# Performance work log

Hardware: AMD Instinct MI355X
Metric: run time of the kernel (lower is better)

Reference implementation:

```python
import jax, jax.numpy as jnp
import numpy as np

B, L, D = 2, 1024, 1024
H = 16
NL = 2
DFF = 4 * D
EPS = 1e-5
W_SCALE = 0.02


def rmsnorm(x, w):
    # x * rsqrt(mean(x^2, -1) + eps) * w   (computed in fp32 as in the torch code)
    xf = x.astype(jnp.float32)
    n = xf * jax.lax.rsqrt(jnp.mean(xf * xf, axis=-1, keepdims=True) + EPS)
    return n.astype(x.dtype) * w


def setup_inputs() -> dict:
    key = jax.random.key(0)
    ks = jax.random.split(key, 10)
    x = jax.random.normal(ks[0], (B, L, D), dtype=jnp.float32)
    # torch nn.Linear weight layout: [out_features, in_features]; y = x @ W.T + b
    qw = jax.random.normal(ks[1], (NL, D, D), dtype=jnp.float32) * W_SCALE
    kw = jax.random.normal(ks[2], (NL, D, D), dtype=jnp.float32) * W_SCALE
    vw = jax.random.normal(ks[3], (NL, D, D), dtype=jnp.float32) * W_SCALE
    ow = jax.random.normal(ks[4], (NL, D, D), dtype=jnp.float32) * W_SCALE
    pn_w = jnp.ones((NL, D), dtype=jnp.float32)
    ln_w = jnp.ones((NL, D), dtype=jnp.float32)
    fc_w = jax.random.normal(ks[5], (NL, DFF, D), dtype=jnp.float32) * W_SCALE
    fc2_w = jax.random.normal(ks[6], (NL, D, DFF), dtype=jnp.float32) * W_SCALE
    fc2_b = jnp.zeros((NL, D), dtype=jnp.float32)
    return {"x": x, "qw": qw, "kw": kw, "vw": vw, "ow": ow,
            "pn_w": pn_w, "ln_w": ln_w, "fc_w": fc_w, "fc2_w": fc2_w, "fc2_b": fc2_b}


def reference(x, qw, kw, vw, ow, pn_w, ln_w, fc_w, fc2_w, fc2_b):
    d = D // H
    for i in range(NL):
        # --- LinearAttention block (dropout=0 -> identity) ---
        h = rmsnorm(x, pn_w[i])                                   # [B,L,D]
        Q = (h @ qw[i].T).reshape(B, L, H, d)
        K = (h @ kw[i].T).reshape(B, L, H, d)
        V = (h @ vw[i].T).reshape(B, L, H, d)
        # outer-product state per position, cumulated over L (causal linear attn)
        W = jnp.einsum('blhd,blhe->blhde', K, V)                  # [B,L,H,d,d]
        W = jnp.cumsum(W, axis=1)
        a = jnp.einsum('blhd,blhde->blhe', Q, W).reshape(B, L, D)
        x = x + a @ ow[i].T
        # --- MLP block ---
        m = rmsnorm(x, ln_w[i])
        f = jax.nn.gelu(m @ fc_w[i].T, approximate=False)         # torch nn.GELU default = exact
        x = x + f @ fc2_w[i].T + fc2_b[i]
    return x
```

## Files before the change

kernel.cpp:

```cpp
#include <hip/hip_runtime.h>

#define BB 2
#define LL 1024
#define DD 1024
#define HH 16
#define HD 64
#define DFFN 4096
#define MM (BB*LL)
#define QS 3072

using u16 = unsigned short;
typedef __bf16 bf16x8 __attribute__((ext_vector_type(8)));
typedef float f32x4 __attribute__((ext_vector_type(4)));

__device__ __forceinline__ float b2f(u16 u) {
  union { unsigned int i; float f; } v; v.i = ((unsigned int)u) << 16; return v.f;
}
__device__ __forceinline__ u16 f2b(float f) {
  union { float f; unsigned int i; } v; v.f = f;
  unsigned int x = v.i;
  return (u16)((x + 0x7fffu + ((x >> 16) & 1u)) >> 16);
}
__device__ __forceinline__ float gelu_exact(float x) {
  return 0.5f * x * (1.0f + erff(x * 0.70710678118654752f));
}
__device__ __forceinline__ void gl2lds16(const void* g, void* l) {
  __builtin_amdgcn_global_load_lds((const __attribute__((address_space(1))) void*)g,
                                   (__attribute__((address_space(3))) void*)l, 16, 0, 0);
}

__global__ __launch_bounds__(256) void castw_kernel(const float* __restrict__ in,
                                                    u16* __restrict__ out, int n8) {
  int i = blockIdx.x * 256 + threadIdx.x;
  if (i >= n8) return;
  const float4 a = reinterpret_cast<const float4*>(in)[2 * i];
  const float4 b = reinterpret_cast<const float4*>(in)[2 * i + 1];
  uint4 o;
  o.x = (unsigned)f2b(a.x) | ((unsigned)f2b(a.y) << 16);
  o.y = (unsigned)f2b(a.z) | ((unsigned)f2b(a.w) << 16);
  o.z = (unsigned)f2b(b.x) | ((unsigned)f2b(b.y) << 16);
  o.w = (unsigned)f2b(b.z) | ((unsigned)f2b(b.w) << 16);
  reinterpret_cast<uint4*>(out)[i] = o;
}
__global__ __launch_bounds__(256) void castw3_kernel(const float* __restrict__ s0,
                                                     const float* __restrict__ s1,
                                                     const float* __restrict__ s2,
                                                     u16* __restrict__ out, int n8) {
  int i = blockIdx.x * 256 + threadIdx.x;
  if (i >= n8) return;
  const float* in = (blockIdx.y == 0) ? s0 : (blockIdx.y == 1) ? s1 : s2;
  u16* dst = out + (size_t)blockIdx.y * n8 * 8;
  const float4 a = reinterpret_cast<const float4*>(in)[2 * i];
  const float4 b = reinterpret_cast<const float4*>(in)[2 * i + 1];
  uint4 o;
  o.x = (unsigned)f2b(a.x) | ((unsigned)f2b(a.y) << 16);
  o.y = (unsigned)f2b(a.z) | ((unsigned)f2b(a.w) << 16);
  o.z = (unsigned)f2b(b.x) | ((unsigned)f2b(b.y) << 16);
  o.w = (unsigned)f2b(b.z) | ((unsigned)f2b(b.w) << 16);
  reinterpret_cast<uint4*>(dst)[i] = o;
}

__global__ __launch_bounds__(256) void init_out_kernel(float* __restrict__ out,
                                                       const float* __restrict__ resid,
                                                       const float* __restrict__ bias) {
  const int i = blockIdx.x * 256 + threadIdx.x;
  float4 v = reinterpret_cast<const float4*>(resid)[i];
  if (bias != nullptr) {
    const float4 bv = *reinterpret_cast<const float4*>(bias + ((i * 4) & (DD - 1)));
    v.x += bv.x; v.y += bv.y; v.z += bv.z; v.w += bv.w;
  }
  reinterpret_cast<float4*>(out)[i] = v;
}

__global__ __launch_bounds__(256) void rmsnorm_kernel(const float* __restrict__ x,
                                                      const float* __restrict__ w,
                                                      u16* __restrict__ out) {
  const int row = blockIdx.x, t = threadIdx.x;
  const float4 v = reinterpret_cast<const float4*>(x + (size_t)row * DD)[t];
  float ss = v.x*v.x + v.y*v.y + v.z*v.z + v.w*v.w;
  #pragma unroll
  for (int o = 32; o > 0; o >>= 1) ss += __shfl_down(ss, o);
  __shared__ float red[4];
  if ((t & 63) == 0) red[t >> 6] = ss;
  __syncthreads();
  const float inv = rsqrtf((red[0] + red[1] + red[2] + red[3]) * (1.0f / DD) + 1e-5f);
  const float4 wv = reinterpret_cast<const float4*>(w)[t];
  ushort4 o;
  o.x = f2b(v.x * inv * wv.x);
  o.y = f2b(v.y * inv * wv.y);
  o.z = f2b(v.z * inv * wv.z);
  o.w = f2b(v.w * inv * wv.w);
  reinterpret_cast<ushort4*>(out + (size_t)row * DD)[t] = o;
}

template<int BM, int BN, int ACT>
__global__ __launch_bounds__((BM/64)*(BN/64)*64)
void mfma_gemm(const u16* __restrict__ A, const u16* __restrict__ Wb,
               u16* __restrict__ Cb, int N, int K) {
  constexpr int WCOLS = BN / 64;
  constexpr int NW = (BM / 64) * WCOLS;
  constexpr int NT = NW * 64;
  constexpr int IA = BM * 4 / NT, IB = BN * 4 / NT;
  __shared__ u16 As[BM * 32];
  __shared__ u16 Bs[BN * 32];
  const int t = threadIdx.x;
  const int lane = t & 63, w = t >> 6;
  const int wm = (w / WCOLS) * 64, wn = (w % WCOLS) * 64;
  const int m0 = blockIdx.y * BM, n0 = blockIdx.x * BN;
  const int fr = lane & 15, fq = lane >> 4;

  f32x4 acc[4][4] = {};
  for (int kt = 0; kt < K; kt += 32) {
    #pragma unroll
    for (int i = 0; i < IA; i++) {
      const int c = i * NT + t;
      gl2lds16(A + (size_t)(m0 + (c >> 2)) * K + kt + (c & 3) * 8, &As[c * 8]);
    }
    #pragma unroll
    for (int i = 0; i < IB; i++) {
      const int c = i * NT + t;
      gl2lds16(Wb + (size_t)(n0 + (c >> 2)) * K + kt + (c & 3) * 8, &Bs[c * 8]);
    }
    __syncthreads();
    bf16x8 af[4], bfv[4];
    #pragma unroll
    for (int i = 0; i < 4; i++)
      af[i] = *reinterpret_cast<const bf16x8*>(&As[(wm + i * 16 + fr) * 32 + fq * 8]);
    #pragma unroll
    for (int j = 0; j < 4; j++)
      bfv[j] = *reinterpret_cast<const bf16x8*>(&Bs[(wn + j * 16 + fr) * 32 + fq * 8]);
    #pragma unroll
    for (int i = 0; i < 4; i++)
      #pragma unroll
      for (int j = 0; j < 4; j++)
        acc[i][j] = __builtin_amdgcn_mfma_f32_16x16x32_bf16(af[i], bfv[j], acc[i][j], 0, 0, 0);
    __syncthreads();
  }

  #pragma unroll
  for (int i = 0; i < 4; i++)
    #pragma unroll
    for (int j = 0; j < 4; j++)
      #pragma unroll
      for (int r = 0; r < 4; r++) {
        const int row = m0 + wm + i * 16 + fq * 4 + r;
        const int col = n0 + wn + j * 16 + fr;
        float val = acc[i][j][r];
        if (ACT == 1) val = gelu_exact(val);
        Cb[(size_t)row * N + col] = f2b(val);
      }
}

template<int SPLIT>
__global__ __launch_bounds__(256)
void mfma_gemm_sk(const u16* __restrict__ A, const u16* __restrict__ Wb,
                  float* __restrict__ Co, int N, int K) {
  constexpr int BM = 128, BN = 128;
  __shared__ u16 As[BM * 32];
  __shared__ u16 Bs[BN * 32];
  const int t = threadIdx.x;
  const int lane = t & 63, w = t >> 6;
  const int wm = (w >> 1) * 64, wn = (w & 1) * 64;
  const int m0 = blockIdx.y * BM, n0 = blockIdx.x * BN;
  const int fr = lane & 15, fq = lane >> 4;
  const int Kc = K / SPLIT, k0 = blockIdx.z * Kc;

  f32x4 acc[4][4] = {};
  for (int kt = k0; kt < k0 + Kc; kt += 32) {
    #pragma unroll
    for (int i = 0; i < 2; i++) {
      const int c = i * 256 + t;
      gl2lds16(A + (size_t)(m0 + (c >> 2)) * K + kt + (c & 3) * 8, &As[c * 8]);
      gl2lds16(Wb + (size_t)(n0 + (c >> 2)) * K + kt + (c & 3) * 8, &Bs[c * 8]);
    }
    __syncthreads();
    bf16x8 af[4], bfv[4];
    #pragma unroll
    for (int i = 0; i < 4; i++)
      af[i] = *reinterpret_cast<const bf16x8*>(&As[(wm + i * 16 + fr) * 32 + fq * 8]);
    #pragma unroll
    for (int j = 0; j < 4; j++)
      bfv[j] = *reinterpret_cast<const bf16x8*>(&Bs[(wn + j * 16 + fr) * 32 + fq * 8]);
    #pragma unroll
    for (int i = 0; i < 4; i++)
      #pragma unroll
      for (int j = 0; j < 4; j++)
        acc[i][j] = __builtin_amdgcn_mfma_f32_16x16x32_bf16(af[i], bfv[j], acc[i][j], 0, 0, 0);
    __syncthreads();
  }

  #pragma unroll
  for (int i = 0; i < 4; i++)
    #pragma unroll
    for (int j = 0; j < 4; j++)
      #pragma unroll
      for (int r = 0; r < 4; r++) {
        const int row = m0 + wm + i * 16 + fq * 4 + r;
        const int col = n0 + wn + j * 16 + fr;
        unsafeAtomicAdd(&Co[(size_t)row * N + col], acc[i][j][r]);
      }
}

__global__ __launch_bounds__(256) void kv_trans(const u16* __restrict__ QKV,
                                                u16* __restrict__ Kt, u16* __restrict__ Vt) {
  __shared__ u16 T[64][72];
  const int tile = blockIdx.x;
  const int h2 = blockIdx.y;
  const int b = blockIdx.z;
  const int h = h2 & 15, which = h2 >> 4;
  const int t = threadIdx.x;
  const int pos = t >> 2, d0 = (t & 3) * 16;
  const u16* src = QKV + ((size_t)(b * LL) + tile * 64 + pos) * QS + 1024 + which * 1024 + h * HD + d0;
  union { uint4 u[2]; u16 s[16]; } pk;
  pk.u[0] = reinterpret_cast<const uint4*>(src)[0];
  pk.u[1] = reinterpret_cast<const uint4*>(src)[1];
  #pragma unroll
  for (int j = 0; j < 16; j++) T[d0 + j][pos] = pk.s[j];
  __syncthreads();
  const int d = t >> 2, p0 = (t & 3) * 16;
  u16* dst = (which ? Vt : Kt) + ((size_t)(b * HH + h) * HD + d) * LL + tile * 64 + p0;
  union { uint4 u[2]; u16 s[16]; } ok;
  #pragma unroll
  for (int j = 0; j < 16; j++) ok.s[j] = T[d][p0 + j];
  reinterpret_cast<uint4*>(dst)[0] = ok.u[0];
  reinterpret_cast<uint4*>(dst)[1] = ok.u[1];
}

__global__ __launch_bounds__(256) void attn_phase1(const u16* __restrict__ QKV,
                                                   const u16* __restrict__ Kt,
                                                   const u16* __restrict__ Vt,
                                                   u16* __restrict__ Oa,
                                                   u16* __restrict__ Slt) {
  __shared__ u16 Ss[4][16][64];
  const int tile = blockIdx.x, h = blockIdx.y, b = blockIdx.z;
  const int t = threadIdx.x, lane = t & 63, w = t >> 6;
  const int fr = lane & 15, fq = lane >> 4;
  const size_t tok0 = (size_t)(b * LL + tile * 64);
  const size_t bh = (size_t)(b * HH + h);
  const u16* Qb  = QKV + tok0 * QS + h * HD;
  const u16* Kb  = Qb + 1024;
  const u16* Ktb = Kt + bh * (HD * LL) + tile * 64;
  const u16* Vtb = Vt + bh * (HD * LL) + tile * 64;

  bf16x8 aq[2], bk[4][2];
  #pragma unroll
  for (int kh = 0; kh < 2; kh++)
    aq[kh] = *reinterpret_cast<const bf16x8*>(Qb + (size_t)(16*w + fr) * QS + kh*32 + fq*8);
  #pragma unroll
  for (int n4 = 0; n4 < 4; n4++)
    #pragma unroll
    for (int kh = 0; kh < 2; kh++)
      bk[n4][kh] = *reinterpret_cast<const bf16x8*>(Kb + (size_t)(16*n4 + fr) * QS + kh*32 + fq*8);
  f32x4 sacc[4] = {};
  #pragma unroll
  for (int n4 = 0; n4 < 4; n4++) {
    sacc[n4] = __builtin_amdgcn_mfma_f32_16x16x32_bf16(aq[0], bk[n4][0], sacc[n4], 0, 0, 0);
    sacc[n4] = __builtin_amdgcn_mfma_f32_16x16x32_bf16(aq[1], bk[n4][1], sacc[n4], 0, 0, 0);
  }
  #pragma unroll
  for (int n4 = 0; n4 < 4; n4++)
    #pragma unroll
    for (int r = 0; r < 4; r++) {
      const bool keep = (16*w + 4*fq + r) >= (16*n4 + fr);
      Ss[w][4*fq + r][16*n4 + fr] = keep ? f2b(sacc[n4][r]) : (u16)0;
    }
  __syncthreads();

  bf16x8 va[2], kt[4][2];
  #pragma unroll
  for (int kh = 0; kh < 2; kh++)
    va[kh] = *reinterpret_cast<const bf16x8*>(Vtb + (size_t)(16*w + fr) * LL + kh*32 + fq*8);
  #pragma unroll
  for (int n4 = 0; n4 < 4; n4++)
    #pragma unroll
    for (int kh = 0; kh < 2; kh++)
      kt[n4][kh] = *reinterpret_cast<const bf16x8*>(Ktb + (size_t)(16*n4 + fr) * LL + kh*32 + fq*8);
  f32x4 lacc[4] = {};
  #pragma unroll
  for (int n4 = 0; n4 < 4; n4++) {
    lacc[n4] = __builtin_amdgcn_mfma_f32_16x16x32_bf16(va[0], kt[n4][0], lacc[n4], 0, 0, 0);
    lacc[n4] = __builtin_amdgcn_mfma_f32_16x16x32_bf16(va[1], kt[n4][1], lacc[n4], 0, 0, 0);
  }
  u16* So = Slt + (bh * 16 + tile) * 4096;
  #pragma unroll
  for (int n4 = 0; n4 < 4; n4++)
    #pragma unroll
    for (int r = 0; r < 4; r++)
      So[(size_t)(16*w + 4*fq + r) * 64 + 16*n4 + fr] = f2b(lacc[n4][r]);

  bf16x8 sa[2], vb[4][2];
  #pragma unroll
  for (int kh = 0; kh < 2; kh++)
    sa[kh] = *reinterpret_cast<const bf16x8*>(&Ss[w][fr][kh*32 + fq*8]);
  #pragma unroll
  for (int n4 = 0; n4 < 4; n4++)
    #pragma unroll
    for (int kh = 0; kh < 2; kh++)
      vb[n4][kh] = *reinterpret_cast<const bf16x8*>(Vtb + (size_t)(16*n4 + fr) * LL + kh*32 + fq*8);
  f32x4 oacc[4] = {};
  #pragma unroll
  for (int n4 = 0; n4 < 4; n4++) {
    oacc[n4] = __builtin_amdgcn_mfma_f32_16x16x32_bf16(sa[0], vb[n4][0], oacc[n4], 0, 0, 0);
    oacc[n4] = __builtin_amdgcn_mfma_f32_16x16x32_bf16(sa[1], vb[n4][1], oacc[n4], 0, 0, 0);
  }
  u16* Ob = Oa + (tok0 + 16*w) * DD + h * HD;
  #pragma unroll
  for (int n4 = 0; n4 < 4; n4++)
    #pragma unroll
    for (int r = 0; r < 4; r++)
      Ob[(size_t)(4*fq + r) * DD + 16*n4 + fr] = f2b(oacc[n4][r]);
}

__global__ __launch_bounds__(256) void attn_phase2(const u16* __restrict__ Slt,
                                                   u16* __restrict__ Wc) {
  const int rg = blockIdx.x, h = blockIdx.y, b = blockIdx.z;
  const size_t base = ((size_t)((b * HH + h) * 16)) * 4096 + rg * 512 + threadIdx.x * 2;
  float r0 = 0.f, r1 = 0.f;
  for (int tl = 0; tl < 16; tl++) {
    const size_t p = base + (size_t)tl * 4096;
    const unsigned d = *reinterpret_cast<const unsigned*>(Slt + p);
    *reinterpret_cast<unsigned*>(Wc + p) = (unsigned)f2b(r0) | ((unsigned)f2b(r1) << 16);
    r0 += b2f((u16)(d & 0xffff));
    r1 += b2f((u16)(d >> 16));
  }
}

__global__ __launch_bounds__(256) void attn_phase3(const u16* __restrict__ QKV,
                                                   const u16* __restrict__ Wc,
                                                   u16* __restrict__ Oa) {
  const int tile = blockIdx.x, h = blockIdx.y, b = blockIdx.z;
  const int t = threadIdx.x, lane = t & 63, w = t >> 6;
  const int fr = lane & 15, fq = lane >> 4;
  const size_t tok0 = (size_t)(b * LL + tile * 64);
  const size_t bh = (size_t)(b * HH + h);
  const u16* Qb = QKV + tok0 * QS + h * HD;
  const u16* Wb = Wc + (bh * 16 + tile) * 4096;

  bf16x8 aq[2], wb[4][2];
  #pragma unroll
  for (int kh = 0; kh < 2; kh++)
    aq[kh] = *reinterpret_cast<const bf16x8*>(Qb + (size_t)(16*w + fr) * QS + kh*32 + fq*8);
  #pragma unroll
  for (int n4 = 0; n4 < 4; n4++)
    #pragma unroll
    for (int kh = 0; kh < 2; kh++)
      wb[n4][kh] = *reinterpret_cast<const bf16x8*>(Wb + (size_t)(16*n4 + fr) * 64 + kh*32 + fq*8);
  f32x4 oacc[4] = {};
  #pragma unroll
  for (int n4 = 0; n4 < 4; n4++) {
    oacc[n4] = __builtin_amdgcn_mfma_f32_16x16x32_bf16(aq[0], wb[n4][0], oacc[n4], 0, 0, 0);
    oacc[n4] = __builtin_amdgcn_mfma_f32_16x16x32_bf16(aq[1], wb[n4][1], oacc[n4], 0, 0, 0);
  }
  u16* Ob = Oa + (tok0 + 16*w) * DD + h * HD;
  #pragma unroll
  for (int n4 = 0; n4 < 4; n4++)
    #pragma unroll
    for (int r = 0; r < 4; r++) {
      const size_t idx = (size_t)(4*fq + r) * DD + 16*n4 + fr;
      Ob[idx] = f2b(b2f(Ob[idx]) + oacc[n4][r]);
    }
}

extern "C" void kernel_launch(void* const* d_in, const int* in_sizes, int n_in,
                              void* d_out, int out_size, void* d_ws, size_t ws_size,
                              hipStream_t stream) {
  const float* x_in = (const float*)d_in[0];
  const float* qw   = (const float*)d_in[1];
  const float* kw   = (const float*)d_in[2];
  const float* vw   = (const float*)d_in[3];
  const float* ow   = (const float*)d_in[4];
  const float* pn   = (const float*)d_in[5];
  const float* ln   = (const float*)d_in[6];
  const float* fcw  = (const float*)d_in[7];
  const float* fc2w = (const float*)d_in[8];
  const float* fc2b = (const float*)d_in[9];

  char* ws = (char*)d_ws;
  u16* wbuf = (u16*)ws;
  u16* slt  = (u16*)ws;
  u16* wcum = (u16*)(ws + (size_t)(4 << 20));
  u16* h    = (u16*)(ws + (size_t)(8 << 20));
  u16* qkv  = (u16*)(ws + (size_t)(12 << 20));
  u16* f    = (u16*)(ws + (size_t)(12 << 20));
  u16* vt   = (u16*)(ws + (size_t)(24 << 20));
  u16* kt   = (u16*)(ws + (size_t)(28 << 20));
  float* xf = (float*)d_out;

  const int n8D = DD * DD / 8;
  const int n8F = DFFN * DD / 8;
  const int gInit = MM * DD / 4 / 256;

  for (int i = 0; i < 2; i++) {
    const float* qwi  = qw   + (size_t)i * DD * DD;
    const float* kwi  = kw   + (size_t)i * DD * DD;
    const float* vwi  = vw   + (size_t)i * DD * DD;
    const float* owi  = ow   + (size_t)i * DD * DD;
    const float* fcwi = fcw  + (size_t)i * DFFN * DD;
    const float* f2wi = fc2w + (size_t)i * DD * DFFN;
    const float* src  = (i == 0) ? x_in : xf;

    rmsnorm_kernel<<<MM, 256, 0, stream>>>(src, pn + i * DD, h);
    castw3_kernel<<<dim3(n8D / 256, 3), 256, 0, stream>>>(qwi, kwi, vwi, wbuf, n8D);
    mfma_gemm<128, 128, 0><<<dim3(QS / 128, MM / 128), 256, 0, stream>>>(
        h, wbuf, qkv, QS, DD);
    kv_trans<<<dim3(16, 32, BB), 256, 0, stream>>>(qkv, kt, vt);
    attn_phase1<<<dim3(16, HH, BB), 256, 0, stream>>>(qkv, kt, vt, h, slt);
    attn_phase2<<<dim3(8, HH, BB), 256, 0, stream>>>(slt, wcum);
    attn_phase3<<<dim3(16, HH, BB), 256, 0, stream>>>(qkv, wcum, h);
    castw_kernel<<<n8D / 256, 256, 0, stream>>>(owi, wbuf, n8D);
    init_out_kernel<<<gInit, 256, 0, stream>>>(xf, src, nullptr);
    mfma_gemm_sk<4><<<dim3(DD / 128, MM / 128, 4), 256, 0, stream>>>(h, wbuf, xf, DD, DD);
    rmsnorm_kernel<<<MM, 256, 0, stream>>>(xf, ln + i * DD, h);
    castw_kernel<<<n8F / 256, 256, 0, stream>>>(fcwi, wbuf, n8F);
    mfma_gemm<128, 128, 1><<<dim3(DFFN / 128, MM / 128), 256, 0, stream>>>(
        h, wbuf, f, DFFN, DD);
    castw_kernel<<<n8F / 256, 256, 0, stream>>>(f2wi, wbuf, n8F);
    float* co = (i == 1) ? (float*)d_out : xf;
    init_out_kernel<<<gInit, 256, 0, stream>>>(co, xf, fc2b + i * DD);
    mfma_gemm_sk<4><<<dim3(DD / 128, MM / 128, 4), 256, 0, stream>>>(f, wbuf, co, DD, DFFN);
  }
}
```

Measured before the change: 547.0 us.

## Fuse fp32 weight cast into GEMMs with double-buffered LDS pipeline

Removes the separate fp32-to-bf16 weight cast kernels. The GEMMs now read fp32 weights directly, convert them in registers and store bf16 into LDS. The main loop becomes double-buffered: the next K-slice of weights is prefetched into registers and A is DMA'd into the alternate LDS buffer while MFMAs run on the current buffer. This saves the cast launches and the extra write/read of bf16 weights, but every output-row tile now re-reads fp32 weights, which doubles weight bytes per load and adds register pressure.

New measurement: 682.3 us. +24.7%, slower.

```diff
diff --git a/kernel.cpp b/kernel.cpp
--- a/kernel.cpp
+++ b/kernel.cpp
@@ -28,36 +28,166 @@
   __builtin_amdgcn_global_load_lds((const __attribute__((address_space(1))) void*)g,
                                    (__attribute__((address_space(3))) void*)l, 16, 0, 0);
 }
-
-__global__ __launch_bounds__(256) void castw_kernel(const float* __restrict__ in,
-                                                    u16* __restrict__ out, int n8) {
-  int i = blockIdx.x * 256 + threadIdx.x;
-  if (i >= n8) return;
-  const float4 a = reinterpret_cast<const float4*>(in)[2 * i];
-  const float4 b = reinterpret_cast<const float4*>(in)[2 * i + 1];
+__device__ __forceinline__ uint4 pack8(const float4& a, const float4& b) {
   uint4 o;
   o.x = (unsigned)f2b(a.x) | ((unsigned)f2b(a.y) << 16);
   o.y = (unsigned)f2b(a.z) | ((unsigned)f2b(a.w) << 16);
   o.z = (unsigned)f2b(b.x) | ((unsigned)f2b(b.y) << 16);
   o.w = (unsigned)f2b(b.z) | ((unsigned)f2b(b.w) << 16);
-  reinterpret_cast<uint4*>(out)[i] = o;
-}
-__global__ __launch_bounds__(256) void castw3_kernel(const float* __restrict__ s0,
-                                                     const float* __restrict__ s1,
-                                                     const float* __restrict__ s2,
-                                                     u16* __restrict__ out, int n8) {
-  int i = blockIdx.x * 256 + threadIdx.x;
-  if (i >= n8) return;
-  const float* in = (blockIdx.y == 0) ? s0 : (blockIdx.y == 1) ? s1 : s2;
-  u16* dst = out + (size_t)blockIdx.y * n8 * 8;
-  const float4 a = reinterpret_cast<const float4*>(in)[2 * i];
-  const float4 b = reinterpret_cast<const float4*>(in)[2 * i + 1];
-  uint4 o;
-  o.x = (unsigned)f2b(a.x) | ((unsigned)f2b(a.y) << 16);
-  o.y = (unsigned)f2b(a.z) | ((unsigned)f2b(a.w) << 16);
-  o.z = (unsigned)f2b(b.x) | ((unsigned)f2b(b.y) << 16);
-  o.w = (unsigned)f2b(b.z) | ((unsigned)f2b(b.w) << 16);
-  reinterpret_cast<uint4*>(dst)[i] = o;
+  return o;
+}
+
+template<int IB, int NT>
+__device__ __forceinline__ void loadW(const float* __restrict__ W, int n0, int K, int kt,
+                                      int t, float4 w[IB][2]) {
+  #pragma unroll
+  for (int i = 0; i < IB; i++) {
+    const int c = i * NT + t;
+    const float* wp = W + (size_t)(n0 + (c >> 2)) * K + kt + (c & 3) * 8;
+    w[i][0] = reinterpret_cast<const float4*>(wp)[0];
+    w[i][1] = reinterpret_cast<const float4*>(wp)[1];
+  }
+}
+template<int IB, int NT>
+__device__ __forceinline__ void cvtW(u16* Bsb, int t, const float4 w[IB][2]) {
+  #pragma unroll
+  for (int i = 0; i < IB; i++) {
+    const int c = i * NT + t;
+    *reinterpret_cast<uint4*>(&Bsb[c * 8]) = pack8(w[i][0], w[i][1]);
+  }
+}
+template<int IA, int NT>
+__device__ __forceinline__ void dmaA(const u16* __restrict__ A, int m0, int K, int kt,
+                                     int t, u16* Asb) {
+  #pragma unroll
+  for (int i = 0; i < IA; i++) {
+    const int c = i * NT + t;
+    gl2lds16(A + (size_t)(m0 + (c >> 2)) * K + kt + (c & 3) * 8, &Asb[c * 8]);
+  }
+}
+__device__ __forceinline__ void mfma_tile(const u16* Asb, const u16* Bsb,
+                                          int wm, int wn, int fr, int fq, f32x4 acc[4][4]) {
+  bf16x8 af[4], bfv[4];
+  #pragma unroll
+  for (int i = 0; i < 4; i++)
+    af[i] = *reinterpret_cast<const bf16x8*>(&Asb[(wm + i * 16 + fr) * 32 + fq * 8]);
+  #pragma unroll
+  for (int j = 0; j < 4; j++)
+    bfv[j] = *reinterpret_cast<const bf16x8*>(&Bsb[(wn + j * 16 + fr) * 32 + fq * 8]);
+  #pragma unroll
+  for (int i = 0; i < 4; i++)
+    #pragma unroll
+    for (int j = 0; j < 4; j++)
+      acc[i][j] = __builtin_amdgcn_mfma_f32_16x16x32_bf16(af[i], bfv[j], acc[i][j], 0, 0, 0);
+}
+
+template<int BM, int BN, int ACT, int QKV3>
+__global__ __launch_bounds__((BM/64)*(BN/64)*64)
+void mfma_gemm(const u16* __restrict__ A, const float* __restrict__ W0,
+               const float* __restrict__ W1, const float* __restrict__ W2,
+               u16* __restrict__ Cb, int N, int K) {
+  constexpr int WCOLS = BN / 64;
+  constexpr int NW = (BM / 64) * WCOLS;
+  constexpr int NT = NW * 64;
+  constexpr int IA = BM * 4 / NT, IB = BN * 4 / NT;
+  __shared__ u16 As[2][BM * 32];
+  __shared__ u16 Bs[2][BN * 32];
+  const int t = threadIdx.x;
+  const int lane = t & 63, w = t >> 6;
+  const int wm = (w / WCOLS) * 64, wn = (w % WCOLS) * 64;
+  const int m0 = blockIdx.y * BM;
+  const int n0out = blockIdx.x * BN;
+  const float* W = W0;
+  int n0 = n0out;
+  if (QKV3) {
+    const int sel = n0out >> 10;
+    W = (sel == 0) ? W0 : (sel == 1) ? W1 : W2;
+    n0 = n0out & 1023;
+  }
+  const int fr = lane & 15, fq = lane >> 4;
+
+  f32x4 acc[4][4] = {};
+  float4 wA[IB][2], wB[IB][2];
+
+  loadW<IB, NT>(W, n0, K, 0, t, wA);
+  dmaA<IA, NT>(A, m0, K, 0, t, &As[0][0]);
+  loadW<IB, NT>(W, n0, K, 32, t, wB);
+  cvtW<IB, NT>(&Bs[0][0], t, wA);
+
+  for (int kt = 0; kt < K; kt += 64) {
+    __syncthreads();
+    if (kt + 64 < K) loadW<IB, NT>(W, n0, K, kt + 64, t, wA);
+    if (kt + 32 < K) dmaA<IA, NT>(A, m0, K, kt + 32, t, &As[1][0]);
+    mfma_tile(&As[0][0], &Bs[0][0], wm, wn, fr, fq, acc);
+    if (kt + 32 < K) cvtW<IB, NT>(&Bs[1][0], t, wB);
+    if (kt + 32 >= K) break;
+    __syncthreads();
+    if (kt + 96 < K) loadW<IB, NT>(W, n0, K, kt + 96, t, wB);
+    if (kt + 64 < K) dmaA<IA, NT>(A, m0, K, kt + 64, t, &As[0][0]);
+    mfma_tile(&As[1][0], &Bs[1][0], wm, wn, fr, fq, acc);
+    if (kt + 64 < K) cvtW<IB, NT>(&Bs[0][0], t, wA);
+  }
+
+  #pragma unroll
+  for (int i = 0; i < 4; i++)
+    #pragma unroll
+    for (int j = 0; j < 4; j++)
+      #pragma unroll
+      for (int r = 0; r < 4; r++) {
+        const int row = m0 + wm + i * 16 + fq * 4 + r;
+        const int col = n0out + wn + j * 16 + fr;
+        float val = acc[i][j][r];
+        if (ACT == 1) val = gelu_exact(val);
+        Cb[(size_t)row * N + col] = f2b(val);
+      }
+}
+
+template<int SPLIT>
+__global__ __launch_bounds__(256)
+void mfma_gemm_sk(const u16* __restrict__ A, const float* __restrict__ W,
+                  float* __restrict__ Co, int N, int K) {
+  constexpr int BM = 128, BN = 128, NT = 256, IA = 2, IB = 2;
+  __shared__ u16 As[2][BM * 32];
+  __shared__ u16 Bs[2][BN * 32];
+  const int t = threadIdx.x;
+  const int lane = t & 63, w = t >> 6;
+  const int wm = (w >> 1) * 64, wn = (w & 1) * 64;
+  const int m0 = blockIdx.y * BM, n0 = blockIdx.x * BN;
+  const int fr = lane & 15, fq = lane >> 4;
+  const int Kc = K / SPLIT, k0 = blockIdx.z * Kc, kend = k0 + Kc;
+
+  f32x4 acc[4][4] = {};
+  float4 wA[IB][2], wB[IB][2];
+
+  loadW<IB, NT>(W, n0, K, k0, t, wA);
+  dmaA<IA, NT>(A, m0, K, k0, t, &As[0][0]);
+  loadW<IB, NT>(W, n0, K, k0 + 32, t, wB);
+  cvtW<IB, NT>(&Bs[0][0], t, wA);
+
+  for (int kt = k0; kt < kend; kt += 64) {
+    __syncthreads();
+    if (kt + 64 < kend) loadW<IB, NT>(W, n0, K, kt + 64, t, wA);
+    if (kt + 32 < kend) dmaA<IA, NT>(A, m0, K, kt + 32, t, &As[1][0]);
+    mfma_tile(&As[0][0], &Bs[0][0], wm, wn, fr, fq, acc);
+    if (kt + 32 < kend) cvtW<IB, NT>(&Bs[1][0], t, wB);
+    if (kt + 32 >= kend) break;
+    __syncthreads();
+    if (kt + 96 < kend) loadW<IB, NT>(W, n0, K, kt + 96, t, wB);
+    if (kt + 64 < kend) dmaA<IA, NT>(A, m0, K, kt + 64, t, &As[0][0]);
+    mfma_tile(&As[1][0], &Bs[1][0], wm, wn, fr, fq, acc);
+    if (kt + 64 < kend) cvtW<IB, NT>(&Bs[0][0], t, wA);
+  }
+
+  #pragma unroll
+  for (int i = 0; i < 4; i++)
+    #pragma unroll
+    for (int j = 0; j < 4; j++)
+      #pragma unroll
+      for (int r = 0; r < 4; r++) {
+        const int row = m0 + wm + i * 16 + fq * 4 + r;
+        const int col = n0 + wn + j * 16 + fr;
+        unsafeAtomicAdd(&Co[(size_t)row * N + col], acc[i][j][r]);
+      }
 }
 
 __global__ __launch_bounds__(256) void init_out_kernel(float* __restrict__ out,
@@ -91,114 +221,6 @@
   o.z = f2b(v.z * inv * wv.z);
   o.w = f2b(v.w * inv * wv.w);
   reinterpret_cast<ushort4*>(out + (size_t)row * DD)[t] = o;
-}
-
-template<int BM, int BN, int ACT>
-__global__ __launch_bounds__((BM/64)*(BN/64)*64)
-void mfma_gemm(const u16* __restrict__ A, const u16* __restrict__ Wb,
-               u16* __restrict__ Cb, int N, int K) {
-  constexpr int WCOLS = BN / 64;
-  constexpr int NW = (BM / 64) * WCOLS;
-  constexpr int NT = NW * 64;
-  constexpr int IA = BM * 4 / NT, IB = BN * 4 / NT;
-  __shared__ u16 As[BM * 32];
-  __shared__ u16 Bs[BN * 32];
-  const int t = threadIdx.x;
-  const int lane = t & 63, w = t >> 6;
-  const int wm = (w / WCOLS) * 64, wn = (w % WCOLS) * 64;
-  const int m0 = blockIdx.y * BM, n0 = blockIdx.x * BN;
-  const int fr = lane & 15, fq = lane >> 4;
-
-  f32x4 acc[4][4] = {};
-  for (int kt = 0; kt < K; kt += 32) {
-    #pragma unroll
-    for (int i = 0; i < IA; i++) {
-      const int c = i * NT + t;
-      gl2lds16(A + (size_t)(m0 + (c >> 2)) * K + kt + (c & 3) * 8, &As[c * 8]);
-    }
-    #pragma unroll
-    for (int i = 0; i < IB; i++) {
-      const int c = i * NT + t;
-      gl2lds16(Wb + (size_t)(n0 + (c >> 2)) * K + kt + (c & 3) * 8, &Bs[c * 8]);
-    }
-    __syncthreads();
-    bf16x8 af[4], bfv[4];
-    #pragma unroll
-    for (int i = 0; i < 4; i++)
-      af[i] = *reinterpret_cast<const bf16x8*>(&As[(wm + i * 16 + fr) * 32 + fq * 8]);
-    #pragma unroll
-    for (int j = 0; j < 4; j++)
-      bfv[j] = *reinterpret_cast<const bf16x8*>(&Bs[(wn + j * 16 + fr) * 32 + fq * 8]);
-    #pragma unroll
-    for (int i = 0; i < 4; i++)
-      #pragma unroll
-      for (int j = 0; j < 4; j++)
-        acc[i][j] = __builtin_amdgcn_mfma_f32_16x16x32_bf16(af[i], bfv[j], acc[i][j], 0, 0, 0);
-    __syncthreads();
-  }
-
-  #pragma unroll
-  for (int i = 0; i < 4; i++)
-    #pragma unroll
-    for (int j = 0; j < 4; j++)
-      #pragma unroll
-      for (int r = 0; r < 4; r++) {
-        const int row = m0 + wm + i * 16 + fq * 4 + r;
-        const int col = n0 + wn + j * 16 + fr;
-        float val = acc[i][j][r];
-        if (ACT == 1) val = gelu_exact(val);
-        Cb[(size_t)row * N + col] = f2b(val);
-      }
-}
-
-template<int SPLIT>
-__global__ __launch_bounds__(256)
-void mfma_gemm_sk(const u16* __restrict__ A, const u16* __restrict__ Wb,
-                  float* __restrict__ Co, int N, int K) {
-  constexpr int BM = 128, BN = 128;
-  __shared__ u16 As[BM * 32];
-  __shared__ u16 Bs[BN * 32];
-  const int t = threadIdx.x;
-  const int lane = t & 63, w = t >> 6;
-  const int wm = (w >> 1) * 64, wn = (w & 1) * 64;
-  const int m0 = blockIdx.y * BM, n0 = blockIdx.x * BN;
-  const int fr = lane & 15, fq = lane >> 4;
-  const int Kc = K / SPLIT, k0 = blockIdx.z * Kc;
-
-  f32x4 acc[4][4] = {};
-  for (int kt = k0; kt < k0 + Kc; kt += 32) {
-    #pragma unroll
-    for (int i = 0; i < 2; i++) {
-      const int c = i * 256 + t;
-      gl2lds16(A + (size_t)(m0 + (c >> 2)) * K + kt + (c & 3) * 8, &As[c * 8]);
-      gl2lds16(Wb + (size_t)(n0 + (c >> 2)) * K + kt + (c & 3) * 8, &Bs[c * 8]);
-    }
-    __syncthreads();
-    bf16x8 af[4], bfv[4];
-    #pragma unroll
-    for (int i = 0; i < 4; i++)
-      af[i] = *reinterpret_cast<const bf16x8*>(&As[(wm + i * 16 + fr) * 32 + fq * 8]);
-    #pragma unroll
-    for (int j = 0; j < 4; j++)
-      bfv[j] = *reinterpret_cast<const bf16x8*>(&Bs[(wn + j * 16 + fr) * 32 + fq * 8]);
-    #pragma unroll
-    for (int i = 0; i < 4; i++)
-      #pragma unroll
-      for (int j = 0; j < 4; j++)
-        acc[i][j] = __builtin_amdgcn_mfma_f32_16x16x32_bf16(af[i], bfv[j], acc[i][j], 0, 0, 0);
-    __syncthreads();
-  }
-
-  #pragma unroll
-  for (int i = 0; i < 4; i++)
-    #pragma unroll
-    for (int j = 0; j < 4; j++)
-      #pragma unroll
-      for (int r = 0; r < 4; r++) {
-        const int row = m0 + wm + i * 16 + fq * 4 + r;
-        const int col = n0 + wn + j * 16 + fr;
-        unsafeAtomicAdd(&Co[(size_t)row * N + col], acc[i][j][r]);
-      }
 }
 
 __global__ __launch_bounds__(256) void kv_trans(const u16* __restrict__ QKV,
@@ -376,7 +398,6 @@
   const float* fc2b = (const float*)d_in[9];
 
   char* ws = (char*)d_ws;
-  u16* wbuf = (u16*)ws;
   u16* slt  = (u16*)ws;
   u16* wcum = (u16*)(ws + (size_t)(4 << 20));
   u16* h    = (u16*)(ws + (size_t)(8 << 20));
@@ -386,8 +407,6 @@
   u16* kt   = (u16*)(ws + (size_t)(28 << 20));
   float* xf = (float*)d_out;
 
-  const int n8D = DD * DD / 8;
-  const int n8F = DFFN * DD / 8;
   const int gInit = MM * DD / 4 / 256;
 
   for (int i = 0; i < 2; i++) {
@@ -400,23 +419,19 @@
     const float* src  = (i == 0) ? x_in : xf;
 
     rmsnorm_kernel<<<MM, 256, 0, stream>>>(src, pn + i * DD, h);
-    castw3_kernel<<<dim3(n8D / 256, 3), 256, 0, stream>>>(qwi, kwi, vwi, wbuf, n8D);
-    mfma_gemm<128, 128, 0><<<dim3(QS / 128, MM / 128), 256, 0, stream>>>(
-        h, wbuf, qkv, QS, DD);
+    mfma_gemm<128, 128, 0, 1><<<dim3(QS / 128, MM / 128), 256, 0, stream>>>(
+        h, qwi, kwi, vwi, qkv, QS, DD);
     kv_trans<<<dim3(16, 32, BB), 256, 0, stream>>>(qkv, kt, vt);
     attn_phase1<<<dim3(16, HH, BB), 256, 0, stream>>>(qkv, kt, vt, h, slt);
     attn_phase2<<<dim3(8, HH, BB), 256, 0, stream>>>(slt, wcum);
     attn_phase3<<<dim3(16, HH, BB), 256, 0, stream>>>(qkv, wcum, h);
-    castw_kernel<<<n8D / 256, 256, 0, stream>>>(owi, wbuf, n8D);
     init_out_kernel<<<gInit, 256, 0, stream>>>(xf, src, nullptr);
-    mfma_gemm_sk<4><<<dim3(DD / 128, MM / 128, 4), 256, 0, stream>>>(h, wbuf, xf, DD, DD);
+    mfma_gemm_sk<4><<<dim3(DD / 128, MM / 128, 4), 256, 0, stream>>>(h, owi, xf, DD, DD);
     rmsnorm_kernel<<<MM, 256, 0, stream>>>(xf, ln + i * DD, h);
-    castw_kernel<<<n8F / 256, 256, 0, stream>>>(fcwi, wbuf, n8F);
-    mfma_gemm<128, 128, 1><<<dim3(DFFN / 128, MM / 128), 256, 0, stream>>>(
-        h, wbuf, f, DFFN, DD);
-    castw_kernel<<<n8F / 256, 256, 0, stream>>>(f2wi, wbuf, n8F);
+    mfma_gemm<128, 128, 1, 0><<<dim3(DFFN / 128, MM / 128), 256, 0, stream>>>(
+        h, fcwi, fcwi, fcwi, f, DFFN, DD);
     float* co = (i == 1) ? (float*)d_out : xf;
     init_out_kernel<<<gInit, 256, 0, stream>>>(co, xf, fc2b + i * DD);
-    mfma_gemm_sk<4><<<dim3(DD / 128, MM / 128, 4), 256, 0, stream>>>(f, wbuf, co, DD, DFFN);
-  }
-}
+    mfma_gemm_sk<4><<<dim3(DD / 128, MM / 128, 4), 256, 0, stream>>>(f, f2wi, co, DD, DFFN);
+  }
+}
```

## Deepen GEMM K-tiles to 64, shrink M tiles, raise fc2 split-K

Applied to the files above, without the earlier changes.

Each GEMM main loop now stages a K-step of 64 instead of 32 into LDS, so there are half as many barrier pairs per unit of work. The QKV and fc1 GEMMs switch to 64x128 tiles with 128 threads, which doubles the block count and improves occupancy across the CUs. The fc2 split-K factor goes from 4 to 8 to add parallelism. In exchange, LDS use per block rises, the wider 128-byte rows may cause more LDS bank conflicts since nothing swizzles them, and fc2 does twice as many atomic adds.

New measurement: 580.8 us. 1.06x slower.

```diff
diff --git a/kernel.cpp b/kernel.cpp
--- a/kernel.cpp
+++ b/kernel.cpp
@@ -93,6 +93,34 @@
   reinterpret_cast<ushort4*>(out + (size_t)row * DD)[t] = o;
 }
 
+template<int ROWS, int NT>
+__device__ __forceinline__ void dma64(const u16* __restrict__ g, int r0, int K, int kt,
+                                      int t, u16* lds) {
+  #pragma unroll
+  for (int i = 0; i < ROWS * 8 / NT; i++) {
+    const int c = i * NT + t;
+    gl2lds16(g + (size_t)(r0 + (c >> 3)) * K + kt + (c & 7) * 8, &lds[c * 8]);
+  }
+}
+__device__ __forceinline__ void mfma_tile64(const u16* Asb, const u16* Bsb,
+                                            int wm, int wn, int fr, int fq, f32x4 acc[4][4]) {
+  #pragma unroll
+  for (int kh = 0; kh < 2; kh++) {
+    bf16x8 af[4], bfv[4];
+    #pragma unroll
+    for (int i = 0; i < 4; i++)
+      af[i] = *reinterpret_cast<const bf16x8*>(&Asb[(wm + i * 16 + fr) * 64 + kh * 32 + fq * 8]);
+    #pragma unroll
+    for (int j = 0; j < 4; j++)
+      bfv[j] = *reinterpret_cast<const bf16x8*>(&Bsb[(wn + j * 16 + fr) * 64 + kh * 32 + fq * 8]);
+    #pragma unroll
+    for (int i = 0; i < 4; i++)
+      #pragma unroll
+      for (int j = 0; j < 4; j++)
+        acc[i][j] = __builtin_amdgcn_mfma_f32_16x16x32_bf16(af[i], bfv[j], acc[i][j], 0, 0, 0);
+  }
+}
+
 template<int BM, int BN, int ACT>
 __global__ __launch_bounds__((BM/64)*(BN/64)*64)
 void mfma_gemm(const u16* __restrict__ A, const u16* __restrict__ Wb,
@@ -100,9 +128,8 @@
   constexpr int WCOLS = BN / 64;
   constexpr int NW = (BM / 64) * WCOLS;
   constexpr int NT = NW * 64;
-  constexpr int IA = BM * 4 / NT, IB = BN * 4 / NT;
-  __shared__ u16 As[BM * 32];
-  __shared__ u16 Bs[BN * 32];
+  __shared__ u16 As[BM * 64];
+  __shared__ u16 Bs[BN * 64];
   const int t = threadIdx.x;
   const int lane = t & 63, w = t >> 6;
   const int wm = (w / WCOLS) * 64, wn = (w % WCOLS) * 64;
@@ -110,30 +137,11 @@
   const int fr = lane & 15, fq = lane >> 4;
 
   f32x4 acc[4][4] = {};
-  for (int kt = 0; kt < K; kt += 32) {
-    #pragma unroll
-    for (int i = 0; i < IA; i++) {
-      const int c = i * NT + t;
-      gl2lds16(A + (size_t)(m0 + (c >> 2)) * K + kt + (c & 3) * 8, &As[c * 8]);
-    }
-    #pragma unroll
-    for (int i = 0; i < IB; i++) {
-      const int c = i * NT + t;
-      gl2lds16(Wb + (size_t)(n0 + (c >> 2)) * K + kt + (c & 3) * 8, &Bs[c * 8]);
-    }
+  for (int kt = 0; kt < K; kt += 64) {
+    dma64<BM, NT>(A, m0, K, kt, t, As);
+    dma64<BN, NT>(Wb, n0, K, kt, t, Bs);
     __syncthreads();
-    bf16x8 af[4], bfv[4];
-    #pragma unroll
-    for (int i = 0; i < 4; i++)
-      af[i] = *reinterpret_cast<const bf16x8*>(&As[(wm + i * 16 + fr) * 32 + fq * 8]);
-    #pragma unroll
-    for (int j = 0; j < 4; j++)
-      bfv[j] = *reinterpret_cast<const bf16x8*>(&Bs[(wn + j * 16 + fr) * 32 + fq * 8]);
-    #pragma unroll
-    for (int i = 0; i < 4; i++)
-      #pragma unroll
-      for (int j = 0; j < 4; j++)
-        acc[i][j] = __builtin_amdgcn_mfma_f32_16x16x32_bf16(af[i], bfv[j], acc[i][j], 0, 0, 0);
+    mfma_tile64(As, Bs, wm, wn, fr, fq, acc);
     __syncthreads();
   }
 
@@ -155,37 +163,22 @@
 __global__ __launch_bounds__(256)
 void mfma_gemm_sk(const u16* __restrict__ A, const u16* __restrict__ Wb,
                   float* __restrict__ Co, int N, int K) {
-  constexpr int BM = 128, BN = 128;
-  __shared__ u16 As[BM * 32];
-  __shared__ u16 Bs[BN * 32];
+  constexpr int BM = 128, BN = 128, NT = 256;
+  __shared__ u16 As[BM * 64];
+  __shared__ u16 Bs[BN * 64];
   const int t = threadIdx.x;
   const int lane = t & 63, w = t >> 6;
   const int wm = (w >> 1) * 64, wn = (w & 1) * 64;
   const int m0 = blockIdx.y * BM, n0 = blockIdx.x * BN;
   const int fr = lane & 15, fq = lane >> 4;
-  const int Kc = K / SPLIT, k0 = blockIdx.z * Kc;
+  const int Kc = K / SPLIT, k0 = blockIdx.z * Kc, kend = k0 + Kc;
 
   f32x4 acc[4][4] = {};
-  for (int kt = k0; kt < k0 + Kc; kt += 32) {
-    #pragma unroll
-    for (int i = 0; i < 2; i++) {
-      const int c = i * 256 + t;
-      gl2lds16(A + (size_t)(m0 + (c >> 2)) * K + kt + (c & 3) * 8, &As[c * 8]);
-      gl2lds16(Wb + (size_t)(n0 + (c >> 2)) * K + kt + (c & 3) * 8, &Bs[c * 8]);
-    }
+  for (int kt = k0; kt < kend; kt += 64) {
+    dma64<BM, NT>(A, m0, K, kt, t, As);
+    dma64<BN, NT>(Wb, n0, K, kt, t, Bs);
     __syncthreads();
-    bf16x8 af[4], bfv[4];
-    #pragma unroll
-    for (int i = 0; i < 4; i++)
-      af[i] = *reinterpret_cast<const bf16x8*>(&As[(wm + i * 16 + fr) * 32 + fq * 8]);
-    #pragma unroll
-    for (int j = 0; j < 4; j++)
-      bfv[j] = *reinterpret_cast<const bf16x8*>(&Bs[(wn + j * 16 + fr) * 32 + fq * 8]);
-    #pragma unroll
-    for (int i = 0; i < 4; i++)
-      #pragma unroll
-      for (int j = 0; j < 4; j++)
-        acc[i][j] = __builtin_amdgcn_mfma_f32_16x16x32_bf16(af[i], bfv[j], acc[i][j], 0, 0, 0);
+    mfma_tile64(As, Bs, wm, wn, fr, fq, acc);
     __syncthreads();
   }
 
@@ -401,7 +394,7 @@
 
     rmsnorm_kernel<<<MM, 256, 0, stream>>>(src, pn + i * DD, h);
     castw3_kernel<<<dim3(n8D / 256, 3), 256, 0, stream>>>(qwi, kwi, vwi, wbuf, n8D);
-    mfma_gemm<128, 128, 0><<<dim3(QS / 128, MM / 128), 256, 0, stream>>>(
+    mfma_gemm<64, 128, 0><<<dim3(QS / 128, MM / 64), 128, 0, stream>>>(
         h, wbuf, qkv, QS, DD);
     kv_trans<<<dim3(16, 32, BB), 256, 0, stream>>>(qkv, kt, vt);
     attn_phase1<<<dim3(16, HH, BB), 256, 0, stream>>>(qkv, kt, vt, h, slt);
@@ -412,11 +405,11 @@
     mfma_gemm_sk<4><<<dim3(DD / 128, MM / 128, 4), 256, 0, stream>>>(h, wbuf, xf, DD, DD);
     rmsnorm_kernel<<<MM, 256, 0, stream>>>(xf, ln + i * DD, h);
     castw_kernel<<<n8F / 256, 256, 0, stream>>>(fcwi, wbuf, n8F);
-    mfma_gemm<128, 128, 1><<<dim3(DFFN / 128, MM / 128), 256, 0, stream>>>(
+    mfma_gemm<64, 128, 1><<<dim3(DFFN / 128, MM / 64), 128, 0, stream>>>(
         h, wbuf, f, DFFN, DD);
     castw_kernel<<<n8F / 256, 256, 0, stream>>>(f2wi, wbuf, n8F);
     float* co = (i == 1) ? (float*)d_out : xf;
     init_out_kernel<<<gInit, 256, 0, stream>>>(co, xf, fc2b + i * DD);
-    mfma_gemm_sk<4><<<dim3(DD / 128, MM / 128, 4), 256, 0, stream>>>(f, wbuf, co, DD, DFFN);
-  }
-}
+    mfma_gemm_sk<8><<<dim3(DD / 128, MM / 128, 8), 256, 0, stream>>>(f, wbuf, co, DD, DFFN);
+  }
+}
```
